# Kernel tuning notes

Measured on AMD Instinct MI355X. Metric: run time of the kernel, lower is better.

Reference implementation:

```python
import jax, jax.numpy as jnp
import numpy as np

TWO_PI = 2.0 * np.pi


def setup_inputs() -> dict:
    key = jax.random.key(0)
    k1, k2 = jax.random.split(key)
    vortex_feature = jax.random.normal(k1, (4, 256, 4), dtype=jnp.float32)
    points = jax.random.normal(k2, (4, 128, 128, 2), dtype=jnp.float32)
    return {"vortex_feature": vortex_feature, "points": points}


def reference(vortex_feature, points):
    # vortex_feature: [B, N, 4] -> y, x, tau, sig
    y, x, tau, sig = jnp.split(vortex_feature, 4, axis=-1)  # each [B, N, 1]
    loc = jnp.concatenate([y, x], axis=-1)                  # [B, N, 2]
    tau = tau[..., 0]                                       # [B, N]
    sig = sig[..., 0]                                       # [B, N]

    # points: [B, H, W, 2] -> pairwise differences [B, H, W, N, 2]
    distances = points[:, :, :, None, :] - loc[:, None, None, :, :]
    sq_distance = jnp.sum(distances ** 2, axis=-1, keepdims=True)  # [B,H,W,N,1]

    src_sigma = sig[:, None, None, :, None]      # [B,1,1,N,1]
    src_strength = tau[:, None, None, :, None]   # [B,1,1,N,1]

    falloff = (1.0 - jnp.exp(-sq_distance / src_sigma ** 2)) / (TWO_PI * sq_distance)
    strength = src_strength * falloff            # [B,H,W,N,1]

    d1 = distances[..., 0]
    d2 = distances[..., 1]
    velocity = strength * jnp.stack([d2, -d1], axis=-1)  # [B,H,W,N,2]
    velocity = jnp.sum(velocity, axis=-2)                # [B,H,W,2]
    return velocity
```

## Files before the change

kernel.cpp:

```cpp
#include <hip/hip_runtime.h>


constexpr int NV = 256;
constexpr int PPB = 16384;
constexpr float INV_2PI = 0.15915494309189535f;

__global__ __launch_bounds__(256) void vortex_vel_kernel(
    const float* __restrict__ vf,
    const float* __restrict__ pts,
    float* __restrict__ out)
{
    const int b = blockIdx.x >> 6;
    const int pbase = (blockIdx.x & 63) << 8;
    const int t = threadIdx.x;

    __shared__ float sy[NV], sx[NV], st[NV], sis[NV];

    {
        const float4 v = reinterpret_cast<const float4*>(vf)[b * NV + t];
        sy[t]  = v.x;
        sx[t]  = v.y;
        st[t]  = v.z * INV_2PI;
        sis[t] = 1.0f / (v.w * v.w);
    }
    __syncthreads();

    const int pidx = b * PPB + pbase + t;
    const float2 p = reinterpret_cast<const float2*>(pts)[pidx];

    float v0 = 0.0f, v1 = 0.0f;
    #pragma unroll 8
    for (int k = 0; k < NV; ++k) {
        const float d0 = p.x - sy[k];
        const float d1 = p.y - sx[k];
        const float sq = d0 * d0 + d1 * d1;
        const float e    = __expf(-sq * sis[k]);
        const float fall = st[k] * (1.0f - e) * __builtin_amdgcn_rcpf(sq);
        v0 = fmaf(fall, d1, v0);
        v1 = fmaf(-fall, d0, v1);
    }

    reinterpret_cast<float2*>(out)[pidx] = make_float2(v0, v1);
}

extern "C" void kernel_launch(void* const* d_in, const int* in_sizes, int n_in,
                              void* d_out, int out_size, void* d_ws, size_t ws_size,
                              hipStream_t stream) {
    const float* vf  = (const float*)d_in[0];
    const float* pts = (const float*)d_in[1];
    float* out = (float*)d_out;

    dim3 grid(256);
    dim3 block(256);
    vortex_vel_kernel<<<grid, block, 0, stream>>>(vf, pts, out);
}
```

Baseline: 14.87 us.

## Split vortex sum across wavefronts with scalar loads and LDS reduction

Each block now handles 64 points, with its four wavefronts each summing over a quarter of the vortices, and the grid grows to 1024 blocks. The vortex data is read directly from global memory with a wave-uniform index so it can go through scalar loads, which removes the shared-memory staging. A small shared-memory reduction then combines the four partial sums. In exchange, each vortex term now computes its sigma reciprocal inline, and the final reduction adds a barrier and leaves half the threads idle during the store.

```diff
diff --git a/kernel.cpp b/kernel.cpp
--- a/kernel.cpp
+++ b/kernel.cpp
@@ -6,51 +6,55 @@
 constexpr float INV_2PI = 0.15915494309189535f;
 
 __global__ __launch_bounds__(256) void vortex_vel_kernel(
-    const float* __restrict__ vf,
-    const float* __restrict__ pts,
+    const float4* __restrict__ vf,
+    const float2* __restrict__ pts,
     float* __restrict__ out)
 {
-    const int b = blockIdx.x >> 6;
-    const int pbase = (blockIdx.x & 63) << 8;
-    const int t = threadIdx.x;
+    const int b     = blockIdx.x >> 8;
+    const int pbase = (blockIdx.x & 255) << 6;
+    const int t     = threadIdx.x;
+    const int lane  = t & 63;
+    const int chunk = __builtin_amdgcn_readfirstlane(t >> 6);
 
-    __shared__ float sy[NV], sx[NV], st[NV], sis[NV];
-
-    {
-        const float4 v = reinterpret_cast<const float4*>(vf)[b * NV + t];
-        sy[t]  = v.x;
-        sx[t]  = v.y;
-        st[t]  = v.z * INV_2PI;
-        sis[t] = 1.0f / (v.w * v.w);
-    }
-    __syncthreads();
-
-    const int pidx = b * PPB + pbase + t;
-    const float2 p = reinterpret_cast<const float2*>(pts)[pidx];
+    const float2 p = pts[b * PPB + pbase + lane];
+    const float4* vfc = vf + b * NV + chunk * 64;
 
     float v0 = 0.0f, v1 = 0.0f;
     #pragma unroll 8
-    for (int k = 0; k < NV; ++k) {
-        const float d0 = p.x - sy[k];
-        const float d1 = p.y - sx[k];
-        const float sq = d0 * d0 + d1 * d1;
-        const float e    = __expf(-sq * sis[k]);
-        const float fall = st[k] * (1.0f - e) * __builtin_amdgcn_rcpf(sq);
-        v0 = fmaf(fall, d1, v0);
-        v1 = fmaf(-fall, d0, v1);
+    for (int k = 0; k < 64; ++k) {
+        const float4 v = vfc[k];
+        const float d0 = p.x - v.x;
+        const float d1 = p.y - v.y;
+        const float sq = fmaf(d0, d0, d1 * d1);
+        const float sig2 = v.w * v.w;
+        const float e = __expf(-sq * __builtin_amdgcn_rcpf(sig2));
+        const float r = __builtin_amdgcn_rcpf(sq);
+        const float w = fmaf(-e, r, r) * v.z;
+        v0 = fmaf(w, d1, v0);
+        v1 = fmaf(-w, d0, v1);
     }
 
-    reinterpret_cast<float2*>(out)[pidx] = make_float2(v0, v1);
+    __shared__ float red[4][64][2];
+    red[chunk][lane][0] = v0;
+    red[chunk][lane][1] = v1;
+    __syncthreads();
+
+    if (t < 128) {
+        const int pt = t >> 1, c = t & 1;
+        const float s = red[0][pt][c] + red[1][pt][c]
+                      + red[2][pt][c] + red[3][pt][c];
+        out[(b * PPB + pbase) * 2 + t] = s * INV_2PI;
+    }
 }
 
 extern "C" void kernel_launch(void* const* d_in, const int* in_sizes, int n_in,
                               void* d_out, int out_size, void* d_ws, size_t ws_size,
                               hipStream_t stream) {
-    const float* vf  = (const float*)d_in[0];
-    const float* pts = (const float*)d_in[1];
+    const float4* vf  = (const float4*)d_in[0];
+    const float2* pts = (const float2*)d_in[1];
     float* out = (float*)d_out;
 
-    dim3 grid(256);
+    dim3 grid(1024);
     dim3 block(256);
     vortex_vel_kernel<<<grid, block, 0, stream>>>(vf, pts, out);
 }
```

After: 13.48 us. 1.1x faster.
